# Kernel tuning notes

Hardware: AMD Instinct MI355X
Metric: run time of the kernel (lower is better)

The kernel has to match this reference:

```python
import jax, jax.numpy as jnp
import numpy as np

PATCH = 16
EPS = 1e-5


def _conv_offsets(x, offset_w, offset_b):
    # offset conv: same kernel/stride/padding as the deform conv
    off = jax.lax.conv_general_dilated(
        x, offset_w, window_strides=(PATCH, PATCH), padding='VALID',
        dimension_numbers=('NCHW', 'OIHW', 'NCHW'))
    return off + offset_b[None, :, None, None]


def _deform_conv(x, offset_w, offset_b, dconv_w):
    B, C, H, W = x.shape
    kh = kw = PATCH
    K = kh * kw
    Ho, Wo = H // PATCH, W // PATCH

    off = _conv_offsets(x, offset_w, offset_b)            # [B, 2K, Ho, Wo]
    # mmcv layout: channels are (dy, dx) pairs per kernel point
    off = off.reshape(B, K, 2, Ho, Wo)
    dy = off[:, :, 0].transpose(0, 2, 3, 1)               # [B, Ho, Wo, K]
    dx = off[:, :, 1].transpose(0, 2, 3, 1)

    ii, jj = jnp.meshgrid(jnp.arange(kh), jnp.arange(kw), indexing='ij')
    ki = ii.reshape(-1).astype(x.dtype)                   # [K]
    kj = jj.reshape(-1).astype(x.dtype)
    base_y = (jnp.arange(Ho, dtype=x.dtype) * PATCH)[:, None] + ki[None, :]  # [Ho, K]
    base_x = (jnp.arange(Wo, dtype=x.dtype) * PATCH)[:, None] + kj[None, :]  # [Wo, K]

    py = base_y[None, :, None, :] + dy                    # [B, Ho, Wo, K]
    px = base_x[None, None, :, :] + dx

    y0 = jnp.floor(py); x0 = jnp.floor(px)
    wy1 = py - y0; wx1 = px - x0
    wy0 = 1.0 - wy1; wx0 = 1.0 - wx1
    y0i = y0.astype(jnp.int32); x0i = x0.astype(jnp.int32)
    y1i = y0i + 1;              x1i = x0i + 1

    xt = x.transpose(0, 2, 3, 1)                          # [B, H, W, C]
    bidx = jnp.arange(B)[:, None, None, None]

    def gather(yi, xi):
        ok = ((yi >= 0) & (yi < H) & (xi >= 0) & (xi < W)).astype(x.dtype)
        v = xt[bidx, jnp.clip(yi, 0, H - 1), jnp.clip(xi, 0, W - 1)]  # [B,Ho,Wo,K,C]
        return v * ok[..., None]

    sampled = (gather(y0i, x0i) * (wy0 * wx0)[..., None]
               + gather(y0i, x1i) * (wy0 * wx1)[..., None]
               + gather(y1i, x0i) * (wy1 * wx0)[..., None]
               + gather(y1i, x1i) * (wy1 * wx1)[..., None])  # [B,Ho,Wo,K,C]

    Wk = dconv_w.reshape(dconv_w.shape[0], C, K)          # [O, C, K]
    out = jnp.einsum('bhwkc,ock->bohw', sampled, Wk)      # [B, O, Ho, Wo]
    return out


def setup_inputs() -> dict:
    key = jax.random.key(0)
    ks = jax.random.split(key, 3)
    B, C, H, W = 64, 3, 224, 224
    O = 768
    x = jax.random.normal(ks[0], (B, C, H, W), jnp.float32)
    # small offset weights -> offsets of O(1) pixel, exercising bilinear path
    offset_w = jax.random.normal(ks[1], (2 * PATCH * PATCH, C, PATCH, PATCH), jnp.float32) * 0.01
    offset_b = jnp.zeros((2 * PATCH * PATCH,), jnp.float32)
    dconv_w = jax.random.normal(ks[2], (O, C, PATCH, PATCH), jnp.float32) * 0.02
    bn_gamma = jnp.ones((O,), jnp.float32)
    bn_beta = jnp.zeros((O,), jnp.float32)
    return {"x": x, "offset_w": offset_w, "offset_b": offset_b,
            "dconv_w": dconv_w, "bn_gamma": bn_gamma, "bn_beta": bn_beta}


def reference(x, offset_w, offset_b, dconv_w, bn_gamma, bn_beta):
    B = x.shape[0]
    y = _deform_conv(x, offset_w, offset_b, dconv_w)      # [B, O, Ho, Wo]
    # BatchNorm2d (training-mode batch stats, biased var) per torch semantics
    mean = jnp.mean(y, axis=(0, 2, 3), keepdims=True)
    var = jnp.mean((y - mean) ** 2, axis=(0, 2, 3), keepdims=True)
    yn = (y - mean) * jax.lax.rsqrt(var + EPS)
    yn = yn * bn_gamma[None, :, None, None] + bn_beta[None, :, None, None]
    ya = jax.nn.gelu(yn, approximate=False)               # nn.GELU default = exact
    O, Ho, Wo = ya.shape[1], ya.shape[2], ya.shape[3]
    return ya.reshape(B, O, Ho * Wo).transpose(0, 2, 1)   # [B, N, embed_dim]
```

## Files before the change

kernel.cpp:

```cpp
#include <hip/hip_runtime.h>
#include <math.h>

#define PATCH 16
#define BATCH 64
#define CIN 3
#define HH 224
#define WW 224
#define NPATCH (BATCH*14*14)
#define KDIM 768
#define NOFF 512
#define NOUT 768
#define KPTS 256
#define EPSF 1e-5f
#define CHW (CIN*HH*WW)
#define HWX (HH*WW)
#define NRB (NPATCH/128)

using short8 = __attribute__((ext_vector_type(8))) short;
using f32x4  = __attribute__((ext_vector_type(4))) float;

#define GLOAD16(g, l) __builtin_amdgcn_global_load_lds( \
    (const __attribute__((address_space(1))) void*)(g), \
    (__attribute__((address_space(3))) void*)(l), 16, 0, 0)

__device__ __forceinline__ unsigned short f2bf(float f) {
    unsigned int u = __float_as_uint(f);
    u = (u + 0x7fffu + ((u >> 16) & 1u)) >> 16;
    return (unsigned short)u;
}
__device__ __forceinline__ float bf2f(unsigned short h) {
    return __uint_as_float(((unsigned int)h) << 16);
}
__device__ __forceinline__ float gelu_exact(float v) {
    return 0.5f * v * (1.0f + erff(v * 0.70710678118654752440f));
}

#define N4X (BATCH*CHW/4)
#define N4W1 (NOFF*KDIM/4)
#define N4W2 (NOUT*KDIM/4)
#define N4ALL (N4X+N4W1+N4W2)

__global__ __launch_bounds__(256) void cvt_all(
    const float* __restrict__ x, const float* __restrict__ w1,
    const float* __restrict__ w2, unsigned short* __restrict__ xbf,
    unsigned short* __restrict__ wbf1, unsigned short* __restrict__ wbf2)
{
    for (int i = blockIdx.x*256 + threadIdx.x; i < N4ALL; i += gridDim.x*256) {
        const float* src; unsigned short* dst; int j;
        if (i < N4X)            { src = x;  dst = xbf;  j = i; }
        else if (i < N4X+N4W1)  { src = w1; dst = wbf1; j = i - N4X; }
        else                    { src = w2; dst = wbf2; j = i - N4X - N4W1; }
        float4 v = ((const float4*)src)[j];
        ((ushort4*)dst)[j] = make_ushort4(f2bf(v.x), f2bf(v.y), f2bf(v.z), f2bf(v.w));
    }
}

__global__ __launch_bounds__(256) void gemm_offsets(
    const unsigned short* __restrict__ xbf, const unsigned short* __restrict__ Bw,
    const float* __restrict__ offb, unsigned short* __restrict__ off)
{
    __shared__ unsigned short lds[3*8192];
    const int t = threadIdx.x;
    const int lane = t & 63;
    const int w = t >> 6, wr = w >> 1, wc = w & 1;

    int bid = blockIdx.x;
    int idx = (bid & 7)*49 + (bid >> 3);
    const int bm = (idx >> 2) * 128, bn = (idx & 3) * 128;

    const int rq = t >> 2;
    const int ksw = (((t & 3) ^ ((t >> 3) & 3)) << 3);

    const unsigned short* aBase0;
    const unsigned short* aBase1;
    {
        int p0 = bm + rq,      b0 = p0/196, r0 = p0%196;
        int p1 = bm + 64 + rq, b1 = p1/196, r1 = p1%196;
        aBase0 = xbf + (size_t)b0*CHW + (size_t)((r0/14)*PATCH)*WW + (size_t)((r0%14)*PATCH);
        aBase1 = xbf + (size_t)b1*CHW + (size_t)((r1/14)*PATCH)*WW + (size_t)((r1%14)*PATCH);
    }
    const unsigned short* bS0 = Bw + (size_t)(bn + rq)*KDIM + ksw;
    const unsigned short* bS1 = Bw + (size_t)(bn + 64 + rq)*KDIM + ksw;

    const int row_a = wr*64 + (lane & 15);
    const int row_b = wc*64 + (lane & 15);
    const int klocs = (((lane >> 4) ^ ((lane >> 1) & 3)) << 3);

#define STG1(slot, k0) do { \
        unsigned short* d = lds + (slot)*8192 + t*8; \
        int e = (k0) + ksw; \
        size_t xo = (size_t)(e >> 8)*HWX + (size_t)((e >> 4) & 15)*WW + (e & 15); \
        GLOAD16(aBase0 + xo, d); \
        GLOAD16(aBase1 + xo, d + 2048); \
        GLOAD16(bS0 + (k0), d + 4096); \
        GLOAD16(bS1 + (k0), d + 6144); \
    } while(0)

    f32x4 acc[4][4] = {};
    STG1(0, 0); STG1(1, 32);
    asm volatile("s_waitcnt vmcnt(4)" ::: "memory");
    __builtin_amdgcn_s_barrier();
#pragma unroll
    for (int it = 0; it < 24; ++it) {
        if (it + 2 < 24) STG1((it+2)%3, (it+2)*32);
        const unsigned short* As_ = lds + (it%3)*8192;
        const unsigned short* Bs_ = As_ + 4096;
        short8 af[4], bv[4];
#pragma unroll
        for (int m = 0; m < 4; ++m) af[m] = *(const short8*)&As_[(row_a + m*16)*32 + klocs];
#pragma unroll
        for (int n = 0; n < 4; ++n) bv[n] = *(const short8*)&Bs_[(row_b + n*16)*32 + klocs];
        __builtin_amdgcn_s_setprio(1);
#pragma unroll
        for (int m = 0; m < 4; ++m)
#pragma unroll
            for (int n = 0; n < 4; ++n)
                acc[m][n] = __builtin_amdgcn_mfma_f32_16x16x32_bf16(af[m], bv[n], acc[m][n], 0, 0, 0);
        __builtin_amdgcn_s_setprio(0);
        if (it < 22) { asm volatile("s_waitcnt vmcnt(4) lgkmcnt(0)" ::: "memory"); __builtin_amdgcn_s_barrier(); }
        else if (it == 22) { asm volatile("s_waitcnt vmcnt(0) lgkmcnt(0)" ::: "memory"); __builtin_amdgcn_s_barrier(); }
    }
#undef STG1

    const int col0 = bn + wc*64 + (lane & 15);
    const int r0 = (lane >> 4) * 4;
#pragma unroll
    for (int m = 0; m < 4; ++m) {
        int grow = bm + wr*64 + m*16 + r0;
#pragma unroll
        for (int n = 0; n < 4; ++n) {
            int gcol = col0 + n*16;
            float bias = offb[gcol];
#pragma unroll
            for (int r = 0; r < 4; ++r)
                off[(size_t)(grow + r)*NOFF + gcol] = f2bf(acc[m][n][r] + bias);
        }
    }
}

__global__ __launch_bounds__(256) void sampler(
    const unsigned short* __restrict__ xbf, const unsigned int* __restrict__ offu,
    unsigned short* __restrict__ A2)
{
    int p = blockIdx.x;
    int k = threadIdx.x;
    int b = p / 196, rem = p % 196;
    int ho = rem / 14, wo = rem % 14;

    unsigned int d2 = offu[(size_t)p*KPTS + k];
    float dy = __uint_as_float((d2 & 0xffffu) << 16);
    float dx = __uint_as_float(d2 & 0xffff0000u);
    float py = (float)(ho*PATCH + (k >> 4)) + dy;
    float px = (float)(wo*PATCH + (k & 15)) + dx;
    float fy = floorf(py), fx = floorf(px);
    float wy1 = py - fy, wx1 = px - fx;
    float wy0 = 1.f - wy1, wx0 = 1.f - wx1;
    int y0 = (int)fy, x0 = (int)fx;
    int y1 = y0 + 1, x1 = x0 + 1;
    bool oky0 = (y0 >= 0) & (y0 < HH);
    bool oky1 = (y1 >= 0) & (y1 < HH);
    bool okx0 = (x0 >= 0) & (x0 < WW);
    bool okx1 = (x1 >= 0) & (x1 < WW);
    int yc0 = min(max(y0, 0), HH-1), yc1 = min(max(y1, 0), HH-1);
    int xc0 = min(max(x0, 0), WW-1), xc1 = min(max(x1, 0), WW-1);
    float w00 = wy0*wx0, w01 = wy0*wx1, w10 = wy1*wx0, w11 = wy1*wx1;

    const unsigned short* xb = xbf + (size_t)b*CHW;
#pragma unroll
    for (int c = 0; c < CIN; ++c) {
        const unsigned short* xc = xb + (size_t)c*HWX;
        float v00 = (oky0 && okx0) ? bf2f(xc[(size_t)yc0*WW + xc0]) : 0.f;
        float v01 = (oky0 && okx1) ? bf2f(xc[(size_t)yc0*WW + xc1]) : 0.f;
        float v10 = (oky1 && okx0) ? bf2f(xc[(size_t)yc1*WW + xc0]) : 0.f;
        float v11 = (oky1 && okx1) ? bf2f(xc[(size_t)yc1*WW + xc1]) : 0.f;
        float v = v00*w00 + v01*w01 + v10*w10 + v11*w11;
        A2[(size_t)p*KDIM + c*KPTS + k] = f2bf(v);
    }
}

__global__ __launch_bounds__(256) void gemm_deform(
    const unsigned short* __restrict__ A, const unsigned short* __restrict__ Bw,
    unsigned short* __restrict__ Cbf, float* __restrict__ psum, float* __restrict__ psq)
{
    __shared__ unsigned short lds[3*8192];
    __shared__ float redS[2][128];
    __shared__ float redQ[2][128];
    const int t = threadIdx.x;
    const int lane = t & 63;
    const int w = t >> 6, wr = w >> 1, wc = w & 1;

    int bid = blockIdx.x;
    int xcd = bid & 7, j = bid >> 3;
    int idx = (xcd < 4) ? xcd*74 + j : 296 + (xcd-4)*73 + j;
    const int rblk = idx / 6;
    const int bm = rblk*128, bn = (idx % 6)*128;

    const int rq = t >> 2;
    const int ksw = (((t & 3) ^ ((t >> 3) & 3)) << 3);

    const unsigned short* aS0 = A + (size_t)(bm + rq)*KDIM + ksw;
    const unsigned short* aS1 = A + (size_t)(bm + 64 + rq)*KDIM + ksw;
    const unsigned short* bS0 = Bw + (size_t)(bn + rq)*KDIM + ksw;
    const unsigned short* bS1 = Bw + (size_t)(bn + 64 + rq)*KDIM + ksw;

    const int row_a = wr*64 + (lane & 15);
    const int row_b = wc*64 + (lane & 15);
    const int klocs = (((lane >> 4) ^ ((lane >> 1) & 3)) << 3);

#define STG2(slot, k0) do { \
        unsigned short* d = lds + (slot)*8192 + t*8; \
        GLOAD16(aS0 + (k0), d); \
        GLOAD16(aS1 + (k0), d + 2048); \
        GLOAD16(bS0 + (k0), d + 4096); \
        GLOAD16(bS1 + (k0), d + 6144); \
    } while(0)

    f32x4 acc[4][4] = {};
    STG2(0, 0); STG2(1, 32);
    asm volatile("s_waitcnt vmcnt(4)" ::: "memory");
    __builtin_amdgcn_s_barrier();
#pragma unroll
    for (int it = 0; it < 24; ++it) {
        if (it + 2 < 24) STG2((it+2)%3, (it+2)*32);
        const unsigned short* As_ = lds + (it%3)*8192;
        const unsigned short* Bs_ = As_ + 4096;
        short8 af[4], bv[4];
#pragma unroll
        for (int m = 0; m < 4; ++m) af[m] = *(const short8*)&As_[(row_a + m*16)*32 + klocs];
#pragma unroll
        for (int n = 0; n < 4; ++n) bv[n] = *(const short8*)&Bs_[(row_b + n*16)*32 + klocs];
        __builtin_amdgcn_s_setprio(1);
#pragma unroll
        for (int m = 0; m < 4; ++m)
#pragma unroll
            for (int n = 0; n < 4; ++n)
                acc[m][n] = __builtin_amdgcn_mfma_f32_16x16x32_bf16(af[m], bv[n], acc[m][n], 0, 0, 0);
        __builtin_amdgcn_s_setprio(0);
        if (it < 22) { asm volatile("s_waitcnt vmcnt(4) lgkmcnt(0)" ::: "memory"); __builtin_amdgcn_s_barrier(); }
        else if (it == 22) { asm volatile("s_waitcnt vmcnt(0) lgkmcnt(0)" ::: "memory"); __builtin_amdgcn_s_barrier(); }
    }
#undef STG2

    float s[4] = {}, q[4] = {};
#pragma unroll
    for (int m = 0; m < 4; ++m)
#pragma unroll
        for (int n = 0; n < 4; ++n)
#pragma unroll
            for (int r = 0; r < 4; ++r) {
                float v = acc[m][n][r];
                s[n] += v; q[n] += v*v;
            }
#pragma unroll
    for (int n = 0; n < 4; ++n) {
        s[n] += __shfl_xor(s[n], 16); q[n] += __shfl_xor(q[n], 16);
        s[n] += __shfl_xor(s[n], 32); q[n] += __shfl_xor(q[n], 32);
    }
    if (lane < 16) {
#pragma unroll
        for (int n = 0; n < 4; ++n) {
            redS[wr][wc*64 + n*16 + lane] = s[n];
            redQ[wr][wc*64 + n*16 + lane] = q[n];
        }
    }
    __syncthreads();

    const int col0 = bn + wc*64 + (lane & 15);
    const int r0 = (lane >> 4) * 4;
#pragma unroll
    for (int m = 0; m < 4; ++m) {
        int grow = bm + wr*64 + m*16 + r0;
#pragma unroll
        for (int n = 0; n < 4; ++n) {
            int gcol = col0 + n*16;
#pragma unroll
            for (int r = 0; r < 4; ++r)
                Cbf[(size_t)(grow + r)*NOUT + gcol] = f2bf(acc[m][n][r]);
        }
    }
    if (t < 128) {
        psum[(size_t)rblk*NOUT + bn + t] = redS[0][t] + redS[1][t];
        psq [(size_t)rblk*NOUT + bn + t] = redQ[0][t] + redQ[1][t];
    }
}

__global__ __launch_bounds__(256) void bn_final(
    const float* __restrict__ psum, const float* __restrict__ psq,
    const float* __restrict__ gamma, const float* __restrict__ beta,
    float* __restrict__ scale, float* __restrict__ shift)
{
    int o = blockIdx.x*256 + threadIdx.x;
    float s = 0.f, q = 0.f;
    for (int i = 0; i < NRB; ++i) {
        s += psum[(size_t)i*NOUT + o];
        q += psq [(size_t)i*NOUT + o];
    }
    float mean = s * (1.0f/(float)NPATCH);
    float var  = q * (1.0f/(float)NPATCH) - mean*mean;
    float inv  = 1.0f / sqrtf(var + EPSF);
    float sc   = gamma[o] * inv;
    scale[o] = sc;
    shift[o] = beta[o] - mean*sc;
}

__global__ __launch_bounds__(256) void norm_gelu(
    const unsigned short* __restrict__ ybf, float* __restrict__ out,
    const float* __restrict__ scale, const float* __restrict__ shift)
{
    __shared__ float ssc[NOUT], ssh[NOUT];
    for (int i = threadIdx.x; i < NOUT; i += 256) { ssc[i] = scale[i]; ssh[i] = shift[i]; }
    __syncthreads();
    const size_t total8 = (size_t)NPATCH * NOUT / 8;
    for (size_t i = (size_t)blockIdx.x*256 + threadIdx.x; i < total8;
         i += (size_t)gridDim.x*256) {
        uint4 v = ((const uint4*)ybf)[i];
        int og = (int)(i % (NOUT/8)) * 8;
        float4 o0, o1;
        o0.x = gelu_exact(__uint_as_float(v.x << 16)        * ssc[og+0] + ssh[og+0]);
        o0.y = gelu_exact(__uint_as_float(v.x & 0xffff0000u)* ssc[og+1] + ssh[og+1]);
        o0.z = gelu_exact(__uint_as_float(v.y << 16)        * ssc[og+2] + ssh[og+2]);
        o0.w = gelu_exact(__uint_as_float(v.y & 0xffff0000u)* ssc[og+3] + ssh[og+3]);
        o1.x = gelu_exact(__uint_as_float(v.z << 16)        * ssc[og+4] + ssh[og+4]);
        o1.y = gelu_exact(__uint_as_float(v.z & 0xffff0000u)* ssc[og+5] + ssh[og+5]);
        o1.z = gelu_exact(__uint_as_float(v.w << 16)        * ssc[og+6] + ssh[og+6]);
        o1.w = gelu_exact(__uint_as_float(v.w & 0xffff0000u)* ssc[og+7] + ssh[og+7]);
        ((float4*)out)[2*i]   = o0;
        ((float4*)out)[2*i+1] = o1;
    }
}

extern "C" void kernel_launch(void* const* d_in, const int* in_sizes, int n_in,
                              void* d_out, int out_size, void* d_ws, size_t ws_size,
                              hipStream_t stream)
{
    const float* x      = (const float*)d_in[0];
    const float* offw   = (const float*)d_in[1];
    const float* offb   = (const float*)d_in[2];
    const float* dconvw = (const float*)d_in[3];
    const float* gamma  = (const float*)d_in[4];
    const float* beta   = (const float*)d_in[5];
    float* out = (float*)d_out;

    const size_t NX  = (size_t)BATCH*CHW;
    const size_t NW1 = (size_t)NOFF*KDIM;
    const size_t NW2 = (size_t)NOUT*KDIM;

    unsigned short* xbf   = (unsigned short*)d_ws;
    unsigned short* wbf1  = xbf  + NX;
    unsigned short* wbf2  = wbf1 + NW1;
    unsigned short* A2    = wbf2 + NW2;
    unsigned short* off   = A2   + (size_t)NPATCH*KDIM;
    unsigned short* ybf   = off  + (size_t)NPATCH*NOFF;
    float* fscratch = (float*)(ybf + (size_t)NPATCH*NOUT);
    float* psum  = fscratch;
    float* psq   = psum + NRB*NOUT;
    float* scale = psq  + NRB*NOUT;
    float* shift = scale + NOUT;

    cvt_all<<<4096, 256, 0, stream>>>(x, offw, dconvw, xbf, wbf1, wbf2);
    gemm_offsets<<<392, 256, 0, stream>>>(xbf, wbf1, offb, off);
    sampler<<<NPATCH, 256, 0, stream>>>(xbf, (const unsigned int*)off, A2);
    gemm_deform<<<588, 256, 0, stream>>>(A2, wbf2, ybf, psum, psq);
    bn_final<<<3, 256, 0, stream>>>(psum, psq, gamma, beta, scale, shift);
    norm_gelu<<<2048, 256, 0, stream>>>(ybf, out, scale, shift);
}
```

Before: 111.5 us.

## Deepen GEMM LDS pipeline to four stages and stage sampler window in LDS

Both GEMM kernels move from a 3-slot to a 4-slot LDS ring, prefetching three k-tiles ahead with adjusted vmcnt waits to hide more global latency. The sampler kernel now loads a 22x22 per-channel input window around each patch into shared memory, using coalesced 32-bit loads for interior patches. Bilinear taps are then read from LDS, with a fallback to global gathers for samples whose offsets fall outside the window. The cost is more LDS per block, which may reduce occupancy, plus an extra barrier and window load in the sampler.

```diff
diff --git a/kernel.cpp b/kernel.cpp
--- a/kernel.cpp
+++ b/kernel.cpp
@@ -59,7 +59,7 @@
     const unsigned short* __restrict__ xbf, const unsigned short* __restrict__ Bw,
     const float* __restrict__ offb, unsigned short* __restrict__ off)
 {
-    __shared__ unsigned short lds[3*8192];
+    __shared__ unsigned short lds[4*8192];
     const int t = threadIdx.x;
     const int lane = t & 63;
     const int w = t >> 6, wr = w >> 1, wc = w & 1;
@@ -97,13 +97,13 @@
     } while(0)
 
     f32x4 acc[4][4] = {};
-    STG1(0, 0); STG1(1, 32);
-    asm volatile("s_waitcnt vmcnt(4)" ::: "memory");
+    STG1(0, 0); STG1(1, 32); STG1(2, 64);
+    asm volatile("s_waitcnt vmcnt(8)" ::: "memory");
     __builtin_amdgcn_s_barrier();
 #pragma unroll
     for (int it = 0; it < 24; ++it) {
-        if (it + 2 < 24) STG1((it+2)%3, (it+2)*32);
-        const unsigned short* As_ = lds + (it%3)*8192;
+        if (it + 3 < 24) STG1((it+3)&3, (it+3)*32);
+        const unsigned short* As_ = lds + (it&3)*8192;
         const unsigned short* Bs_ = As_ + 4096;
         short8 af[4], bv[4];
 #pragma unroll
@@ -117,7 +117,8 @@
             for (int n = 0; n < 4; ++n)
                 acc[m][n] = __builtin_amdgcn_mfma_f32_16x16x32_bf16(af[m], bv[n], acc[m][n], 0, 0, 0);
         __builtin_amdgcn_s_setprio(0);
-        if (it < 22) { asm volatile("s_waitcnt vmcnt(4) lgkmcnt(0)" ::: "memory"); __builtin_amdgcn_s_barrier(); }
+        if (it <= 20)      { asm volatile("s_waitcnt vmcnt(8) lgkmcnt(0)" ::: "memory"); __builtin_amdgcn_s_barrier(); }
+        else if (it == 21) { asm volatile("s_waitcnt vmcnt(4) lgkmcnt(0)" ::: "memory"); __builtin_amdgcn_s_barrier(); }
         else if (it == 22) { asm volatile("s_waitcnt vmcnt(0) lgkmcnt(0)" ::: "memory"); __builtin_amdgcn_s_barrier(); }
     }
 #undef STG1
@@ -142,10 +143,33 @@
     const unsigned short* __restrict__ xbf, const unsigned int* __restrict__ offu,
     unsigned short* __restrict__ A2)
 {
+    __shared__ unsigned short win[3][22][24];
     int p = blockIdx.x;
     int k = threadIdx.x;
     int b = p / 196, rem = p % 196;
     int ho = rem / 14, wo = rem % 14;
+    const int gy0 = ho*PATCH - 2, gx0 = wo*PATCH - 2;
+    const unsigned short* xb = xbf + (size_t)b*CHW;
+
+    bool interior = (ho >= 1) && (ho <= 12) && (wo >= 1) && (wo <= 12);
+    if (interior) {
+        for (int idx = k; idx < 3*22*11; idx += 256) {
+            int c = idx / 242, r2 = idx - c*242;
+            int row = r2 / 11, u = r2 - row*11;
+            const unsigned int* src = (const unsigned int*)
+                (xb + (size_t)c*HWX + (size_t)(gy0+row)*WW + gx0);
+            *(unsigned int*)&win[c][row][2*u] = src[u];
+        }
+    } else {
+        for (int idx = k; idx < 3*22*22; idx += 256) {
+            int c = idx / 484, r2 = idx - c*484;
+            int row = r2 / 22, col = r2 - row*22;
+            int gy = min(max(gy0+row, 0), HH-1);
+            int gx = min(max(gx0+col, 0), WW-1);
+            win[c][row][col] = xb[(size_t)c*HWX + (size_t)gy*WW + gx];
+        }
+    }
+    __syncthreads();
 
     unsigned int d2 = offu[(size_t)p*KPTS + k];
     float dy = __uint_as_float((d2 & 0xffffu) << 16);
@@ -161,20 +185,36 @@
     bool oky1 = (y1 >= 0) & (y1 < HH);
     bool okx0 = (x0 >= 0) & (x0 < WW);
     bool okx1 = (x1 >= 0) & (x1 < WW);
-    int yc0 = min(max(y0, 0), HH-1), yc1 = min(max(y1, 0), HH-1);
-    int xc0 = min(max(x0, 0), WW-1), xc1 = min(max(x1, 0), WW-1);
     float w00 = wy0*wx0, w01 = wy0*wx1, w10 = wy1*wx0, w11 = wy1*wx1;
 
-    const unsigned short* xb = xbf + (size_t)b*CHW;
-#pragma unroll
-    for (int c = 0; c < CIN; ++c) {
-        const unsigned short* xc = xb + (size_t)c*HWX;
-        float v00 = (oky0 && okx0) ? bf2f(xc[(size_t)yc0*WW + xc0]) : 0.f;
-        float v01 = (oky0 && okx1) ? bf2f(xc[(size_t)yc0*WW + xc1]) : 0.f;
-        float v10 = (oky1 && okx0) ? bf2f(xc[(size_t)yc1*WW + xc0]) : 0.f;
-        float v11 = (oky1 && okx1) ? bf2f(xc[(size_t)yc1*WW + xc1]) : 0.f;
-        float v = v00*w00 + v01*w01 + v10*w10 + v11*w11;
-        A2[(size_t)p*KDIM + c*KPTS + k] = f2bf(v);
+    int ry = y0 - gy0, rx = x0 - gx0;
+    if (ry >= 0 && ry <= 20 && rx >= 0 && rx <= 20) {
+        float m00 = oky0 && okx0 ? 1.f : 0.f;
+        float m01 = oky0 && okx1 ? 1.f : 0.f;
+        float m10 = oky1 && okx0 ? 1.f : 0.f;
+        float m11 = oky1 && okx1 ? 1.f : 0.f;
+#pragma unroll
+        for (int c = 0; c < CIN; ++c) {
+            float v00 = bf2f(win[c][ry  ][rx  ]) * m00;
+            float v01 = bf2f(win[c][ry  ][rx+1]) * m01;
+            float v10 = bf2f(win[c][ry+1][rx  ]) * m10;
+            float v11 = bf2f(win[c][ry+1][rx+1]) * m11;
+            float v = v00*w00 + v01*w01 + v10*w10 + v11*w11;
+            A2[(size_t)p*KDIM + c*KPTS + k] = f2bf(v);
+        }
+    } else {
+        int yc0 = min(max(y0, 0), HH-1), yc1 = min(max(y1, 0), HH-1);
+        int xc0 = min(max(x0, 0), WW-1), xc1 = min(max(x1, 0), WW-1);
+#pragma unroll
+        for (int c = 0; c < CIN; ++c) {
+            const unsigned short* xc = xb + (size_t)c*HWX;
+            float v00 = (oky0 && okx0) ? bf2f(xc[(size_t)yc0*WW + xc0]) : 0.f;
+            float v01 = (oky0 && okx1) ? bf2f(xc[(size_t)yc0*WW + xc1]) : 0.f;
+            float v10 = (oky1 && okx0) ? bf2f(xc[(size_t)yc1*WW + xc0]) : 0.f;
+            float v11 = (oky1 && okx1) ? bf2f(xc[(size_t)yc1*WW + xc1]) : 0.f;
+            float v = v00*w00 + v01*w01 + v10*w10 + v11*w11;
+            A2[(size_t)p*KDIM + c*KPTS + k] = f2bf(v);
+        }
     }
 }
 
@@ -182,7 +222,7 @@
     const unsigned short* __restrict__ A, const unsigned short* __restrict__ Bw,
     unsigned short* __restrict__ Cbf, float* __restrict__ psum, float* __restrict__ psq)
 {
-    __shared__ unsigned short lds[3*8192];
+    __shared__ unsigned short lds[4*8192];
     __shared__ float redS[2][128];
     __shared__ float redQ[2][128];
     const int t = threadIdx.x;
@@ -216,13 +256,13 @@
     } while(0)
 
     f32x4 acc[4][4] = {};
-    STG2(0, 0); STG2(1, 32);
-    asm volatile("s_waitcnt vmcnt(4)" ::: "memory");
+    STG2(0, 0); STG2(1, 32); STG2(2, 64);
+    asm volatile("s_waitcnt vmcnt(8)" ::: "memory");
     __builtin_amdgcn_s_barrier();
 #pragma unroll
     for (int it = 0; it < 24; ++it) {
-        if (it + 2 < 24) STG2((it+2)%3, (it+2)*32);
-        const unsigned short* As_ = lds + (it%3)*8192;
+        if (it + 3 < 24) STG2((it+3)&3, (it+3)*32);
+        const unsigned short* As_ = lds + (it&3)*8192;
         const unsigned short* Bs_ = As_ + 4096;
         short8 af[4], bv[4];
 #pragma unroll
@@ -236,7 +276,8 @@
             for (int n = 0; n < 4; ++n)
                 acc[m][n] = __builtin_amdgcn_mfma_f32_16x16x32_bf16(af[m], bv[n], acc[m][n], 0, 0, 0);
         __builtin_amdgcn_s_setprio(0);
-        if (it < 22) { asm volatile("s_waitcnt vmcnt(4) lgkmcnt(0)" ::: "memory"); __builtin_amdgcn_s_barrier(); }
+        if (it <= 20)      { asm volatile("s_waitcnt vmcnt(8) lgkmcnt(0)" ::: "memory"); __builtin_amdgcn_s_barrier(); }
+        else if (it == 21) { asm volatile("s_waitcnt vmcnt(4) lgkmcnt(0)" ::: "memory"); __builtin_amdgcn_s_barrier(); }
         else if (it == 22) { asm volatile("s_waitcnt vmcnt(0) lgkmcnt(0)" ::: "memory"); __builtin_amdgcn_s_barrier(); }
     }
 #undef STG2
```

After: 103.6 us. 1.08x faster.
